# Kernel tuning notes

Measured on AMD Instinct MI355X. Metric: run time of the kernel, lower is better.

## Reference

```python
import jax, jax.numpy as jnp
import numpy as np

MASK_ID = 3
MAX_SEN = 128
SEN_DIM = 128
EMBED = 1024


def setup_inputs() -> dict:
    key = jax.random.key(0)
    ks = jax.random.split(key, 12)
    B, S, E, D = 8, 8192, EMBED, SEN_DIM
    s = 0.02
    return {
        "input_ids": jax.random.randint(ks[0], (B, S), 0, 64),
        "hidden_states": jax.random.normal(ks[1], (B, S, E), jnp.float32),
        "Wv": jax.random.normal(ks[2], (E, D), jnp.float32) * s,
        "bv": jnp.zeros((D,), jnp.float32),
        "Wq": jax.random.normal(ks[3], (E, D), jnp.float32) * s,
        "bq": jnp.zeros((D,), jnp.float32),
        "Wk": jax.random.normal(ks[4], (D, D), jnp.float32) * s,
        "bk": jnp.zeros((D,), jnp.float32),
        "Wvt": jax.random.normal(ks[5], (D, D), jnp.float32) * s,
        "bvt": jnp.zeros((D,), jnp.float32),
        "Wo": jax.random.normal(ks[6], (D, E), jnp.float32) * s,
        "bo": jnp.zeros((E,), jnp.float32),
    }


def reference(input_ids, hidden_states, Wv, bv, Wq, bq, Wk, bk, Wvt, bvt, Wo, bo):
    B, S, E = hidden_states.shape
    dt = hidden_states.dtype

    # sentence segmentation: each mask token t with running count c belongs to bucket c-1
    mask = input_ids == MASK_ID                               # (B, S)
    csum = jnp.cumsum(mask.astype(jnp.int32), axis=1)         # (B, S)
    # tokens that are not mask tokens (or overflow max_sen_num) go to dummy bucket MAX_SEN
    seg = jnp.where(mask & (csum <= MAX_SEN), csum - 1, MAX_SEN)  # (B, S)

    # segment-sum replacement for torch.bmm(sen_pos_mask, hidden_states)
    b_idx = jnp.arange(B)[:, None]
    pooled = jnp.zeros((B, MAX_SEN + 1, E), dt).at[b_idx, seg].add(hidden_states)[:, :MAX_SEN]  # (B, M, E)

    static_sen_states = pooled @ Wv + bv                      # (B, M, 128)

    q_token = (hidden_states @ Wq + bq) * (SEN_DIM ** -0.5)   # (B, S, 128)
    k_sen = static_sen_states @ Wk + bk                       # (B, M, 128)
    v_sen = static_sen_states @ Wvt + bvt                     # (B, M, 128)

    # token t may attend to sentences 0..csum[t]-1
    tmp_mask = (jnp.arange(MAX_SEN)[None, None, :] + 1) <= csum[:, :, None]  # (B, S, M)
    neg = jnp.finfo(dt).min
    logits = jnp.einsum('bsd,bmd->bsm', q_token, k_sen) + jnp.where(tmp_mask, jnp.zeros((), dt), neg)
    attn = jax.nn.softmax(logits, axis=-1) * tmp_mask.astype(dt)  # (B, S, M)

    sen_attn_output = jnp.einsum('bsm,bmd->bsd', attn, v_sen) @ Wo + bo  # (B, S, E)
    return sen_attn_output
```

## Files before the change

kernel.cpp:

```cpp
#include <hip/hip_runtime.h>
#include <hip/hip_bf16.h>

#define MASK_ID 3
#define MAX_SEN 128
#define NB 8
#define SEQ 8192
#define EMB 1024
#define DIM 128

typedef __attribute__((ext_vector_type(8))) short short8v;
typedef __attribute__((ext_vector_type(4))) float f32x4;

#define MFMA(a, b, c) __builtin_amdgcn_mfma_f32_16x16x32_bf16(a, b, c, 0, 0, 0)

__device__ __forceinline__ short f2b(float x) {
    union { float f; unsigned u; } v; v.f = x;
    unsigned r = (v.u + 0x7FFFu + ((v.u >> 16) & 1u)) >> 16;
    return (short)r;
}

__device__ __forceinline__ unsigned cvtpk(float a, float b) {
    unsigned r;
    asm("v_cvt_pk_bf16_f32 %0, %1, %2" : "=v"(r) : "v"(a), "v"(b));
    return r;
}

__global__ __launch_bounds__(1024) void seg_kernel(const int* __restrict__ ids,
                                                   int* __restrict__ pos,
                                                   int* __restrict__ nvis) {
    int b = blockIdx.x;
    int tid = threadIdx.x;
    __shared__ int sc[1024];
    __shared__ int sc2[1024];
    const int PER = SEQ / 1024;
    int base = b * SEQ + tid * PER;

    int ids_l[PER];
    int cnt = 0;
    #pragma unroll
    for (int j = 0; j < PER; j++) {
        ids_l[j] = ids[base + j];
        cnt += (ids_l[j] == MASK_ID) ? 1 : 0;
    }
    if (tid < MAX_SEN) pos[b * MAX_SEN + tid] = -1;
    sc[tid] = cnt;
    __syncthreads();

    int* src = sc;
    int* dst = sc2;
    for (int off = 1; off < 1024; off <<= 1) {
        int v = src[tid];
        if (tid >= off) v += src[tid - off];
        dst[tid] = v;
        __syncthreads();
        int* t = src; src = dst; dst = t;
    }
    int incl = src[tid];
    int run = incl - cnt;

    #pragma unroll
    for (int j = 0; j < PER; j++) {
        if (ids_l[j] == MASK_ID) {
            run++;
            if (run <= MAX_SEN) pos[b * MAX_SEN + run - 1] = tid * PER + j;
        }
        int nv = run; if (nv > MAX_SEN) nv = MAX_SEN;
        nvis[base + j] = nv;
    }
}

__global__ __launch_bounds__(256) void prep_w(const float* __restrict__ Wq,
                                              const float* __restrict__ Wo,
                                              short* __restrict__ WqTt,
                                              short* __restrict__ WoTt) {
    int t = blockIdx.x * 256 + threadIdx.x;
    {
        int fid = t >> 6, lp = t & 63;
        int c = fid >> 4, ks = (fid >> 3) & 1, cf = fid & 7;
        int e0 = c * 64 + ks * 32 + (lp >> 4) * 8;
        int d = cf * 16 + (lp & 15);
        short8v v;
        #pragma unroll
        for (int j = 0; j < 8; j++) v[j] = f2b(Wq[(size_t)(e0 + j) * 128 + d]);
        *(short8v*)(WqTt + fid * 512 + lp * 8) = v;
    }
    {
        int fid = t >> 6, lp = t & 63;
        int ef = fid >> 2, kk = fid & 3;
        int e = ef * 16 + (lp & 15);
        int dd0 = kk * 32 + (lp >> 4) * 8;
        short8v v;
        #pragma unroll
        for (int j = 0; j < 8; j++) v[j] = f2b(Wo[(size_t)(dd0 + j) * 1024 + e]);
        *(short8v*)(WoTt + fid * 512 + lp * 8) = v;
    }
}

__global__ __launch_bounds__(128) void statkv_kernel(const float* __restrict__ hidden,
                                                     const float* __restrict__ Wv, const float* __restrict__ bv,
                                                     const float* __restrict__ Wk, const float* __restrict__ bk,
                                                     const float* __restrict__ Wvt, const float* __restrict__ bvt,
                                                     const int* __restrict__ pos,
                                                     short* __restrict__ k_t, short* __restrict__ vT_t) {
    int mg = blockIdx.x;
    int b  = blockIdx.y;
    int d  = threadIdx.x;
    __shared__ float h[4][1024];
    __shared__ float st[4][128];
    int m0 = mg * 4;

    #pragma unroll
    for (int j = 0; j < 4; j++) {
        int p = pos[b * MAX_SEN + m0 + j];
        const float* hp = hidden + ((size_t)b * SEQ + (p < 0 ? 0 : p)) * EMB;
        #pragma unroll
        for (int ii = 0; ii < 2; ii++) {
            float4 v = {0.f, 0.f, 0.f, 0.f};
            if (p >= 0) v = *(const float4*)(hp + ii * 512 + d * 4);
            *(float4*)&h[j][ii * 512 + d * 4] = v;
        }
    }
    __syncthreads();

    float a0 = 0.f, a1 = 0.f, a2 = 0.f, a3 = 0.f;
    for (int e = 0; e < 1024; e += 4) {
        float w0 = Wv[(size_t)e * 128 + d];
        float w1 = Wv[(size_t)(e + 1) * 128 + d];
        float w2 = Wv[(size_t)(e + 2) * 128 + d];
        float w3 = Wv[(size_t)(e + 3) * 128 + d];
        float4 h0 = *(const float4*)&h[0][e];
        float4 h1 = *(const float4*)&h[1][e];
        float4 h2 = *(const float4*)&h[2][e];
        float4 h3 = *(const float4*)&h[3][e];
        a0 += h0.x * w0 + h0.y * w1 + h0.z * w2 + h0.w * w3;
        a1 += h1.x * w0 + h1.y * w1 + h1.z * w2 + h1.w * w3;
        a2 += h2.x * w0 + h2.y * w1 + h2.z * w2 + h2.w * w3;
        a3 += h3.x * w0 + h3.y * w1 + h3.z * w2 + h3.w * w3;
    }
    float bvd = bv[d];
    st[0][d] = bvd + a0;
    st[1][d] = bvd + a1;
    st[2][d] = bvd + a2;
    st[3][d] = bvd + a3;
    __syncthreads();

    float k0 = 0.f, k1 = 0.f, k2 = 0.f, k3 = 0.f;
    float v0 = 0.f, v1 = 0.f, v2 = 0.f, v3 = 0.f;
    for (int e = 0; e < 128; e += 4) {
        float wk0 = Wk[(e) * 128 + d],     wk1 = Wk[(e + 1) * 128 + d];
        float wk2 = Wk[(e + 2) * 128 + d], wk3 = Wk[(e + 3) * 128 + d];
        float wv0 = Wvt[(e) * 128 + d],     wv1 = Wvt[(e + 1) * 128 + d];
        float wv2 = Wvt[(e + 2) * 128 + d], wv3 = Wvt[(e + 3) * 128 + d];
        float4 s0 = *(const float4*)&st[0][e];
        float4 s1 = *(const float4*)&st[1][e];
        float4 s2 = *(const float4*)&st[2][e];
        float4 s3 = *(const float4*)&st[3][e];
        k0 += s0.x * wk0 + s0.y * wk1 + s0.z * wk2 + s0.w * wk3;
        k1 += s1.x * wk0 + s1.y * wk1 + s1.z * wk2 + s1.w * wk3;
        k2 += s2.x * wk0 + s2.y * wk1 + s2.z * wk2 + s2.w * wk3;
        k3 += s3.x * wk0 + s3.y * wk1 + s3.z * wk2 + s3.w * wk3;
        v0 += s0.x * wv0 + s0.y * wv1 + s0.z * wv2 + s0.w * wv3;
        v1 += s1.x * wv0 + s1.y * wv1 + s1.z * wv2 + s1.w * wv3;
        v2 += s2.x * wv0 + s2.y * wv1 + s2.z * wv2 + s2.w * wv3;
        v3 += s3.x * wv0 + s3.y * wv1 + s3.z * wv2 + s3.w * wv3;
    }
    float kv[4] = {k0, k1, k2, k3};
    float vv[4] = {v0, v1, v2, v3};
    float bkd = bk[d], bvtd = bvt[d];
    #pragma unroll
    for (int j = 0; j < 4; j++) {
        int m = m0 + j;
        int kk = d >> 5, lq = (d >> 3) & 3, jj = d & 7;
        int fid = (m >> 4) * 4 + kk;
        k_t[(b << 14) + fid * 512 + (lq * 16 + (m & 15)) * 8 + jj] = f2b(bkd + kv[j]);
        int df = d >> 4, kk2 = m >> 5, lq2 = (m >> 3) & 3, j2 = m & 7;
        int fid2 = df * 4 + kk2;
        vT_t[(b << 14) + fid2 * 512 + (lq2 * 16 + (d & 15)) * 8 + j2] = f2b(bvtd + vv[j]);
    }
}

__global__ __launch_bounds__(256, 3) void attn_kernel(
    const float* __restrict__ hidden,
    const short* __restrict__ WqTt, const float* __restrict__ bq,
    const short* __restrict__ k_t, const short* __restrict__ vT_t,
    const short* __restrict__ WoTt, const float* __restrict__ bo,
    const int* __restrict__ nvis,
    float* __restrict__ out) {
    int wg = (blockIdx.x & 7) * 128 + (blockIdx.x >> 3);
    int b  = wg >> 7;
    int s0 = (wg & 127) * 64;
    int tid = threadIdx.x;
    int lane = tid & 63;
    int w  = tid >> 6;
    int lr = lane & 15;
    int lq = lane >> 4;

    __shared__ __align__(16) char SH[49152];
    char* Ab  = SH;
    char* pPc = SH;
    char* odc = SH + 16384;
    char* qPc = SH + 32768;

    const size_t hrow = (size_t)b * SEQ + s0;
    f32x4 zero = {0.f, 0.f, 0.f, 0.f};

    f32x4 acc[4][2];
    #pragma unroll
    for (int rf = 0; rf < 4; rf++) { acc[rf][0] = zero; acc[rf][1] = zero; }

    int rsub = tid >> 4;
    int cfl  = (tid & 15) * 4;
    const float* hA0 = hidden + (hrow + 0 * 16 + rsub) * EMB + cfl;
    const float* hA1 = hidden + (hrow + 1 * 16 + rsub) * EMB + cfl;
    const float* hA2 = hidden + (hrow + 2 * 16 + rsub) * EMB + cfl;
    const float* hA3 = hidden + (hrow + 3 * 16 + rsub) * EMB + cfl;
    int swzA = (rsub & 7) << 4;
    int dA0 = (0 * 16 + rsub) * 128 + (((tid & 15) * 8) ^ swzA);
    int dA1 = (1 * 16 + rsub) * 128 + (((tid & 15) * 8) ^ swzA);
    int dA2 = (2 * 16 + rsub) * 128 + (((tid & 15) * 8) ^ swzA);
    int dA3 = (3 * 16 + rsub) * 128 + (((tid & 15) * 8) ^ swzA);

    float4 pa0[4], pa1[4], pa2[4];
    short8v Wa[4], Wb[4];

#define LOADA(C, PA) do { \
    PA[0] = *(const float4*)(hA0 + (C) * 64); \
    PA[1] = *(const float4*)(hA1 + (C) * 64); \
    PA[2] = *(const float4*)(hA2 + (C) * 64); \
    PA[3] = *(const float4*)(hA3 + (C) * 64); } while (0)

#define LOADW(C, W) do { \
    const short* wp = WqTt + ((C) * 16 + 2 * w) * 512 + lane * 8; \
    W[0] = *(const short8v*)(wp); \
    W[1] = *(const short8v*)(wp + 512); \
    W[2] = *(const short8v*)(wp + 8 * 512); \
    W[3] = *(const short8v*)(wp + 9 * 512); } while (0)

#define STORE_A(PA) do { \
    unsigned long long v0_ = (unsigned long long)cvtpk(PA[0].z, PA[0].w) << 32 | cvtpk(PA[0].x, PA[0].y); \
    unsigned long long v1_ = (unsigned long long)cvtpk(PA[1].z, PA[1].w) << 32 | cvtpk(PA[1].x, PA[1].y); \
    unsigned long long v2_ = (unsigned long long)cvtpk(PA[2].z, PA[2].w) << 32 | cvtpk(PA[2].x, PA[2].y); \
    unsigned long long v3_ = (unsigned long long)cvtpk(PA[3].z, PA[3].w) << 32 | cvtpk(PA[3].x, PA[3].y); \
    *(unsigned long long*)(Ab + dA0) = v0_; \
    *(unsigned long long*)(Ab + dA1) = v1_; \
    *(unsigned long long*)(Ab + dA2) = v2_; \
    *(unsigned long long*)(Ab + dA3) = v3_; } while (0)

#define COMPUTE(W) do { \
    _Pragma("unroll") \
    for (int ks = 0; ks < 2; ks++) { \
        _Pragma("unroll") \
        for (int rf = 0; rf < 4; rf++) { \
            int row = rf * 16 + lr; \
            short8v fa = *(short8v*)(Ab + ((row * 128 + ks * 64 + lq * 16) ^ ((row & 7) << 4))); \
            acc[rf][0] = MFMA(fa, W[ks * 2 + 0], acc[rf][0]); \
            acc[rf][1] = MFMA(fa, W[ks * 2 + 1], acc[rf][1]); \
        } } } while (0)

#define ITER(c, PA, WW, DO_A, DO_W) do { \
    __builtin_amdgcn_s_barrier();                  \
    STORE_A(PA);                                   \
    if (DO_A) LOADA((c) + 3, PA); \
    asm volatile("s_waitcnt lgkmcnt(0)" ::: "memory"); \
    __builtin_amdgcn_sched_barrier(0); \
    __builtin_amdgcn_s_barrier();                  \
    COMPUTE(WW);                                   \
    if (DO_W) LOADW((c) + 2, WW);                  \
    } while (0)

    LOADW(0, Wa);
    LOADW(1, Wb);
    LOADA(0, pa0);
    LOADA(1, pa1);
    LOADA(2, pa2);

    ITER(0,  pa0, Wa, 1, 1);
    ITER(1,  pa1, Wb, 1, 1);
    ITER(2,  pa2, Wa, 1, 1);
    ITER(3,  pa0, Wb, 1, 1);
    ITER(4,  pa1, Wa, 1, 1);
    ITER(5,  pa2, Wb, 1, 1);
    ITER(6,  pa0, Wa, 1, 1);
    ITER(7,  pa1, Wb, 1, 1);
    ITER(8,  pa2, Wa, 1, 1);
    ITER(9,  pa0, Wb, 1, 1);
    ITER(10, pa1, Wa, 1, 1);
    ITER(11, pa2, Wb, 1, 1);
    ITER(12, pa0, Wa, 1, 1);
    ITER(13, pa1, Wb, 0, 1);
    ITER(14, pa2, Wa, 0, 0);
    ITER(15, pa0, Wb, 0, 0);

    {
        const float scale = 0.08838834764831845f;
        int d0 = w * 32 + lr;
        float bq0 = bq[d0], bq1 = bq[d0 + 16];
        #pragma unroll
        for (int rf = 0; rf < 4; rf++)
            #pragma unroll
            for (int r = 0; r < 4; r++) {
                int row = rf * 16 + lq * 4 + r;
                int x = (row & 7) << 4;
                *(short*)(qPc + row * 256 + ((d0 * 2) ^ x))        = f2b((acc[rf][0][r] + bq0) * scale);
                *(short*)(qPc + row * 256 + (((d0 + 16) * 2) ^ x)) = f2b((acc[rf][1][r] + bq1) * scale);
            }
    }
    __syncthreads();

    {
        f32x4 l[4][2];
        #pragma unroll
        for (int rf = 0; rf < 4; rf++) { l[rf][0] = zero; l[rf][1] = zero; }
        const short* kbase = k_t + (b << 14) + (2 * w) * 4 * 512 + lane * 8;
        #pragma unroll
        for (int kk = 0; kk < 4; kk++) {
            const short8v fb0 = *(const short8v*)(kbase + kk * 512);
            const short8v fb1 = *(const short8v*)(kbase + (4 + kk) * 512);
            #pragma unroll
            for (int rf = 0; rf < 4; rf++) {
                int row = rf * 16 + lr;
                int x = (row & 7) << 4;
                short8v fa = *(short8v*)(qPc + row * 256 + ((kk * 64 + lq * 16) ^ x));
                l[rf][0] = MFMA(fa, fb0, l[rf][0]);
                l[rf][1] = MFMA(fa, fb1, l[rf][1]);
            }
        }
        #pragma unroll
        for (int rf = 0; rf < 4; rf++)
            #pragma unroll
            for (int r = 0; r < 4; r++) {
                int row = rf * 16 + lq * 4 + r;
                int x = (row & 7) << 4;
                *(float*)(SH + row * 512 + (((w * 32 + lr) * 4) ^ x))      = l[rf][0][r];
                *(float*)(SH + row * 512 + (((w * 32 + 16 + lr) * 4) ^ x)) = l[rf][1][r];
            }
    }
    __syncthreads();

    {
        int t = tid >> 2, sub = tid & 3;
        int nv = nvis[b * SEQ + s0 + t];
        int x = (t & 7) << 4;
        float pv[32];
        #pragma unroll
        for (int u = 0; u < 8; u++) {
            float4 v = *(const float4*)(SH + t * 512 + ((sub * 128 + u * 16) ^ x));
            pv[u * 4]     = v.x; pv[u * 4 + 1] = v.y;
            pv[u * 4 + 2] = v.z; pv[u * 4 + 3] = v.w;
        }
        int base_m = sub * 32;
        float mx = -3.0e38f;
        #pragma unroll
        for (int i = 0; i < 32; i++)
            mx = (base_m + i < nv) ? fmaxf(mx, pv[i]) : mx;
        mx = fmaxf(mx, __shfl_xor(mx, 1));
        mx = fmaxf(mx, __shfl_xor(mx, 2));
        float sum = 0.f;
        #pragma unroll
        for (int i = 0; i < 32; i++) {
            float e = (base_m + i < nv) ? __expf(pv[i] - mx) : 0.f;
            pv[i] = e;
            sum += e;
        }
        sum += __shfl_xor(sum, 1);
        sum += __shfl_xor(sum, 2);
        float inv = (nv > 0) ? 1.0f / sum : 0.f;

        __syncthreads();

        #pragma unroll
        for (int u = 0; u < 4; u++) {
            union { short8v s; unsigned uu[4]; } p;
            #pragma unroll
            for (int i = 0; i < 4; i++)
                p.uu[i] = cvtpk(pv[u * 8 + 2 * i] * inv, pv[u * 8 + 2 * i + 1] * inv);
            *(short8v*)(pPc + t * 256 + ((sub * 64 + u * 16) ^ x)) = p.s;
        }
    }
    __syncthreads();

    {
        f32x4 o[4][2];
        #pragma unroll
        for (int rf = 0; rf < 4; rf++) { o[rf][0] = zero; o[rf][1] = zero; }
        const short* vbase = vT_t + (b << 14) + (2 * w) * 4 * 512 + lane * 8;
        #pragma unroll
        for (int kk = 0; kk < 4; kk++) {
            const short8v fb0 = *(const short8v*)(vbase + kk * 512);
            const short8v fb1 = *(const short8v*)(vbase + (4 + kk) * 512);
            #pragma unroll
            for (int rf = 0; rf < 4; rf++) {
                int row = rf * 16 + lr;
                int x = (row & 7) << 4;
                short8v fa = *(short8v*)(pPc + row * 256 + ((kk * 64 + lq * 16) ^ x));
                o[rf][0] = MFMA(fa, fb0, o[rf][0]);
                o[rf][1] = MFMA(fa, fb1, o[rf][1]);
            }
        }
        int d0 = w * 32 + lr;
        #pragma unroll
        for (int rf = 0; rf < 4; rf++)
            #pragma unroll
            for (int r = 0; r < 4; r++) {
                int row = rf * 16 + lq * 4 + r;
                int x = (row & 7) << 4;
                *(short*)(odc + row * 256 + ((d0 * 2) ^ x))        = f2b(o[rf][0][r]);
                *(short*)(odc + row * 256 + (((d0 + 16) * 2) ^ x)) = f2b(o[rf][1][r]);
            }
    }
    __syncthreads();

    {
        short8v af[4][4];
        #pragma unroll
        for (int rf = 0; rf < 4; rf++)
            #pragma unroll
            for (int kk = 0; kk < 4; kk++) {
                int row = rf * 16 + lr;
                int x = (row & 7) << 4;
                af[rf][kk] = *(short8v*)(odc + row * 256 + ((kk * 64 + lq * 16) ^ x));
            }
        __syncthreads();

        float* cst = (float*)SH;
        int srow2 = tid >> 4;
        int scidx = (tid & 15) * 4;

        #pragma unroll
        for (int grp = 0; grp < 4; grp++) {
            f32x4 ac[4][4];
            #pragma unroll
            for (int rf = 0; rf < 4; rf++)
                #pragma unroll
                for (int cf = 0; cf < 4; cf++) ac[rf][cf] = zero;
            #pragma unroll
            for (int kk = 0; kk < 4; kk++) {
                #pragma unroll
                for (int cf = 0; cf < 4; cf++) {
                    const short8v bb = *(const short8v*)(WoTt
                        + ((grp * 16 + w * 4 + cf) * 4 + kk) * 512 + lane * 8);
                    #pragma unroll
                    for (int rf = 0; rf < 4; rf++)
                        ac[rf][cf] = MFMA(af[rf][kk], bb, ac[rf][cf]);
                }
            }
            #pragma unroll
            for (int rf = 0; rf < 4; rf++) {
                #pragma unroll
                for (int cf = 0; cf < 4; cf++)
                    #pragma unroll
                    for (int r = 0; r < 4; r++)
                        cst[(lq * 4 + r) * 260 + w * 64 + cf * 16 + lr] = ac[rf][cf][r];
                __syncthreads();
                #pragma unroll
                for (int i = 0; i < 4; i++) {
                    int cidx = scidx + i * 64;
                    float4 v = *(const float4*)(cst + srow2 * 260 + cidx);
                    float4 b4 = *(const float4*)(bo + grp * 256 + cidx);
                    v.x += b4.x; v.y += b4.y; v.z += b4.z; v.w += b4.w;
                    *(float4*)(&out[(hrow + rf * 16 + srow2) * EMB + grp * 256 + cidx]) = v;
                }
                __syncthreads();
            }
        }
    }
}

extern "C" void kernel_launch(void* const* d_in, const int* in_sizes, int n_in,
                              void* d_out, int out_size, void* d_ws, size_t ws_size,
                              hipStream_t stream) {
    const int*   ids    = (const int*)d_in[0];
    const float* hidden = (const float*)d_in[1];
    const float* Wv     = (const float*)d_in[2];
    const float* bv     = (const float*)d_in[3];
    const float* Wq     = (const float*)d_in[4];
    const float* bq     = (const float*)d_in[5];
    const float* Wk     = (const float*)d_in[6];
    const float* bk     = (const float*)d_in[7];
    const float* Wvt    = (const float*)d_in[8];
    const float* bvt    = (const float*)d_in[9];
    const float* Wo     = (const float*)d_in[10];
    const float* bo     = (const float*)d_in[11];

    char* ws = (char*)d_ws;
    int*   pos   = (int*)ws;
    int*   nvis  = (int*)(ws + (4 << 10));
    short* k_t   = (short*)(ws + (260 << 10));
    short* vT_t  = (short*)(ws + (516 << 10));
    short* WqTt  = (short*)(ws + (772 << 10));
    short* WoTt  = (short*)(ws + (1028 << 10));

    seg_kernel<<<NB, 1024, 0, stream>>>(ids, pos, nvis);
    prep_w<<<64, 256, 0, stream>>>(Wq, Wo, WqTt, WoTt);
    dim3 g2(32, NB);
    statkv_kernel<<<g2, 128, 0, stream>>>(hidden, Wv, bv, Wk, bk, Wvt, bvt, pos, k_t, vT_t);
    attn_kernel<<<NB * (SEQ / 64), 256, 0, stream>>>(hidden, WqTt, bq, k_t, vT_t, WoTt, bo,
                                                     nvis, (float*)d_out);
}
```

Before: 217.2 us.

## Merge seg/prep kernels, widen statkv rows, triple-buffer Q-projection LDS tiles

Folds the weight-conversion kernel into the segmentation kernel with extra blocks, which saves one launch. The statkv kernel now handles 8 sentences per block instead of 4, halving its grid and reusing each weight load across more rows. In the attention kernel, the Q-projection A tile moves from a single LDS buffer to three rotating buffers with one barrier per iteration instead of two. This gives more prefetch distance and less synchronisation, at the cost of more LDS and more register pressure.

```diff
diff --git a/kernel.cpp b/kernel.cpp
--- a/kernel.cpp
+++ b/kernel.cpp
@@ -25,74 +25,75 @@
     return r;
 }
 
-__global__ __launch_bounds__(1024) void seg_kernel(const int* __restrict__ ids,
-                                                   int* __restrict__ pos,
-                                                   int* __restrict__ nvis) {
-    int b = blockIdx.x;
-    int tid = threadIdx.x;
+__global__ __launch_bounds__(1024) void seg_prep_kernel(const int* __restrict__ ids,
+                                                        int* __restrict__ pos,
+                                                        int* __restrict__ nvis,
+                                                        const float* __restrict__ Wq,
+                                                        const float* __restrict__ Wo,
+                                                        short* __restrict__ WqTt,
+                                                        short* __restrict__ WoTt) {
     __shared__ int sc[1024];
     __shared__ int sc2[1024];
-    const int PER = SEQ / 1024;
-    int base = b * SEQ + tid * PER;
-
-    int ids_l[PER];
-    int cnt = 0;
-    #pragma unroll
-    for (int j = 0; j < PER; j++) {
-        ids_l[j] = ids[base + j];
-        cnt += (ids_l[j] == MASK_ID) ? 1 : 0;
-    }
-    if (tid < MAX_SEN) pos[b * MAX_SEN + tid] = -1;
-    sc[tid] = cnt;
-    __syncthreads();
-
-    int* src = sc;
-    int* dst = sc2;
-    for (int off = 1; off < 1024; off <<= 1) {
-        int v = src[tid];
-        if (tid >= off) v += src[tid - off];
-        dst[tid] = v;
+    int tid = threadIdx.x;
+    if (blockIdx.x < 8) {
+        int b = blockIdx.x;
+        const int PER = SEQ / 1024;
+        int base = b * SEQ + tid * PER;
+
+        int ids_l[PER];
+        int cnt = 0;
+        #pragma unroll
+        for (int j = 0; j < PER; j++) {
+            ids_l[j] = ids[base + j];
+            cnt += (ids_l[j] == MASK_ID) ? 1 : 0;
+        }
+        if (tid < MAX_SEN) pos[b * MAX_SEN + tid] = -1;
+        sc[tid] = cnt;
         __syncthreads();
-        int* t = src; src = dst; dst = t;
-    }
-    int incl = src[tid];
-    int run = incl - cnt;
-
-    #pragma unroll
-    for (int j = 0; j < PER; j++) {
-        if (ids_l[j] == MASK_ID) {
-            run++;
-            if (run <= MAX_SEN) pos[b * MAX_SEN + run - 1] = tid * PER + j;
-        }
-        int nv = run; if (nv > MAX_SEN) nv = MAX_SEN;
-        nvis[base + j] = nv;
-    }
-}
-
-__global__ __launch_bounds__(256) void prep_w(const float* __restrict__ Wq,
-                                              const float* __restrict__ Wo,
-                                              short* __restrict__ WqTt,
-                                              short* __restrict__ WoTt) {
-    int t = blockIdx.x * 256 + threadIdx.x;
-    {
-        int fid = t >> 6, lp = t & 63;
-        int c = fid >> 4, ks = (fid >> 3) & 1, cf = fid & 7;
-        int e0 = c * 64 + ks * 32 + (lp >> 4) * 8;
-        int d = cf * 16 + (lp & 15);
-        short8v v;
-        #pragma unroll
-        for (int j = 0; j < 8; j++) v[j] = f2b(Wq[(size_t)(e0 + j) * 128 + d]);
-        *(short8v*)(WqTt + fid * 512 + lp * 8) = v;
-    }
-    {
-        int fid = t >> 6, lp = t & 63;
-        int ef = fid >> 2, kk = fid & 3;
-        int e = ef * 16 + (lp & 15);
-        int dd0 = kk * 32 + (lp >> 4) * 8;
-        short8v v;
-        #pragma unroll
-        for (int j = 0; j < 8; j++) v[j] = f2b(Wo[(size_t)(dd0 + j) * 1024 + e]);
-        *(short8v*)(WoTt + fid * 512 + lp * 8) = v;
+
+        int* src = sc;
+        int* dst = sc2;
+        for (int off = 1; off < 1024; off <<= 1) {
+            int v = src[tid];
+            if (tid >= off) v += src[tid - off];
+            dst[tid] = v;
+            __syncthreads();
+            int* t = src; src = dst; dst = t;
+        }
+        int incl = src[tid];
+        int run = incl - cnt;
+
+        #pragma unroll
+        for (int j = 0; j < PER; j++) {
+            if (ids_l[j] == MASK_ID) {
+                run++;
+                if (run <= MAX_SEN) pos[b * MAX_SEN + run - 1] = tid * PER + j;
+            }
+            int nv = run; if (nv > MAX_SEN) nv = MAX_SEN;
+            nvis[base + j] = nv;
+        }
+    } else {
+        int t = (blockIdx.x - 8) * 1024 + tid;
+        {
+            int fid = t >> 6, lp = t & 63;
+            int c = fid >> 4, ks = (fid >> 3) & 1, cf = fid & 7;
+            int e0 = c * 64 + ks * 32 + (lp >> 4) * 8;
+            int d = cf * 16 + (lp & 15);
+            short8v v;
+            #pragma unroll
+            for (int j = 0; j < 8; j++) v[j] = f2b(Wq[(size_t)(e0 + j) * 128 + d]);
+            *(short8v*)(WqTt + fid * 512 + lp * 8) = v;
+        }
+        {
+            int fid = t >> 6, lp = t & 63;
+            int ef = fid >> 2, kk = fid & 3;
+            int e = ef * 16 + (lp & 15);
+            int dd0 = kk * 32 + (lp >> 4) * 8;
+            short8v v;
+            #pragma unroll
+            for (int j = 0; j < 8; j++) v[j] = f2b(Wo[(size_t)(dd0 + j) * 1024 + e]);
+            *(short8v*)(WoTt + fid * 512 + lp * 8) = v;
+        }
     }
 }
 
@@ -105,12 +106,12 @@
     int mg = blockIdx.x;
     int b  = blockIdx.y;
     int d  = threadIdx.x;
-    __shared__ float h[4][1024];
-    __shared__ float st[4][128];
-    int m0 = mg * 4;
-
-    #pragma unroll
-    for (int j = 0; j < 4; j++) {
+    __shared__ float h[8][1024];
+    __shared__ float st[8][128];
+    int m0 = mg * 8;
+
+    #pragma unroll
+    for (int j = 0; j < 8; j++) {
         int p = pos[b * MAX_SEN + m0 + j];
         const float* hp = hidden + ((size_t)b * SEQ + (p < 0 ? 0 : p)) * EMB;
         #pragma unroll
@@ -122,53 +123,41 @@
     }
     __syncthreads();
 
-    float a0 = 0.f, a1 = 0.f, a2 = 0.f, a3 = 0.f;
+    float a[8];
+    #pragma unroll
+    for (int j = 0; j < 8; j++) a[j] = 0.f;
     for (int e = 0; e < 1024; e += 4) {
         float w0 = Wv[(size_t)e * 128 + d];
         float w1 = Wv[(size_t)(e + 1) * 128 + d];
         float w2 = Wv[(size_t)(e + 2) * 128 + d];
         float w3 = Wv[(size_t)(e + 3) * 128 + d];
-        float4 h0 = *(const float4*)&h[0][e];
-        float4 h1 = *(const float4*)&h[1][e];
-        float4 h2 = *(const float4*)&h[2][e];
-        float4 h3 = *(const float4*)&h[3][e];
-        a0 += h0.x * w0 + h0.y * w1 + h0.z * w2 + h0.w * w3;
-        a1 += h1.x * w0 + h1.y * w1 + h1.z * w2 + h1.w * w3;
-        a2 += h2.x * w0 + h2.y * w1 + h2.z * w2 + h2.w * w3;
-        a3 += h3.x * w0 + h3.y * w1 + h3.z * w2 + h3.w * w3;
+        #pragma unroll
+        for (int j = 0; j < 8; j++) {
+            float4 hj = *(const float4*)&h[j][e];
+            a[j] += hj.x * w0 + hj.y * w1 + hj.z * w2 + hj.w * w3;
+        }
     }
     float bvd = bv[d];
-    st[0][d] = bvd + a0;
-    st[1][d] = bvd + a1;
-    st[2][d] = bvd + a2;
-    st[3][d] = bvd + a3;
-    __syncthreads();
-
-    float k0 = 0.f, k1 = 0.f, k2 = 0.f, k3 = 0.f;
-    float v0 = 0.f, v1 = 0.f, v2 = 0.f, v3 = 0.f;
-    for (int e = 0; e < 128; e += 4) {
-        float wk0 = Wk[(e) * 128 + d],     wk1 = Wk[(e + 1) * 128 + d];
-        float wk2 = Wk[(e + 2) * 128 + d], wk3 = Wk[(e + 3) * 128 + d];
-        float wv0 = Wvt[(e) * 128 + d],     wv1 = Wvt[(e + 1) * 128 + d];
-        float wv2 = Wvt[(e + 2) * 128 + d], wv3 = Wvt[(e + 3) * 128 + d];
-        float4 s0 = *(const float4*)&st[0][e];
-        float4 s1 = *(const float4*)&st[1][e];
-        float4 s2 = *(const float4*)&st[2][e];
-        float4 s3 = *(const float4*)&st[3][e];
-        k0 += s0.x * wk0 + s0.y * wk1 + s0.z * wk2 + s0.w * wk3;
-        k1 += s1.x * wk0 + s1.y * wk1 + s1.z * wk2 + s1.w * wk3;
-        k2 += s2.x * wk0 + s2.y * wk1 + s2.z * wk2 + s2.w * wk3;
-        k3 += s3.x * wk0 + s3.y * wk1 + s3.z * wk2 + s3.w * wk3;
-        v0 += s0.x * wv0 + s0.y * wv1 + s0.z * wv2 + s0.w * wv3;
-        v1 += s1.x * wv0 + s1.y * wv1 + s1.z * wv2 + s1.w * wv3;
-        v2 += s2.x * wv0 + s2.y * wv1 + s2.z * wv2 + s2.w * wv3;
-        v3 += s3.x * wv0 + s3.y * wv1 + s3.z * wv2 + s3.w * wv3;
-    }
-    float kv[4] = {k0, k1, k2, k3};
-    float vv[4] = {v0, v1, v2, v3};
+    #pragma unroll
+    for (int j = 0; j < 8; j++) st[j][d] = bvd + a[j];
+    __syncthreads();
+
+    float kv[8], vv[8];
+    #pragma unroll
+    for (int j = 0; j < 8; j++) { kv[j] = 0.f; vv[j] = 0.f; }
+    for (int e = 0; e < 128; e += 2) {
+        float wk0 = Wk[(e) * 128 + d],  wk1 = Wk[(e + 1) * 128 + d];
+        float wv0 = Wvt[(e) * 128 + d], wv1 = Wvt[(e + 1) * 128 + d];
+        #pragma unroll
+        for (int j = 0; j < 8; j++) {
+            float s0 = st[j][e], s1 = st[j][e + 1];
+            kv[j] += s0 * wk0 + s1 * wk1;
+            vv[j] += s0 * wv0 + s1 * wv1;
+        }
+    }
     float bkd = bk[d], bvtd = bvt[d];
     #pragma unroll
-    for (int j = 0; j < 4; j++) {
+    for (int j = 0; j < 8; j++) {
         int m = m0 + j;
         int kk = d >> 5, lq = (d >> 3) & 3, jj = d & 7;
         int fid = (m >> 4) * 4 + kk;
@@ -196,7 +185,9 @@
     int lq = lane >> 4;
 
     __shared__ __align__(16) char SH[49152];
-    char* Ab  = SH;
+    char* Ab0 = SH;
+    char* Ab1 = SH + 8192;
+    char* Ab2 = SH + 16384;
     char* pPc = SH;
     char* odc = SH + 16384;
     char* qPc = SH + 32768;
@@ -236,35 +227,34 @@
     W[2] = *(const short8v*)(wp + 8 * 512); \
     W[3] = *(const short8v*)(wp + 9 * 512); } while (0)
 
-#define STORE_A(PA) do { \
+#define STORE_A(PA, AB) do { \
     unsigned long long v0_ = (unsigned long long)cvtpk(PA[0].z, PA[0].w) << 32 | cvtpk(PA[0].x, PA[0].y); \
     unsigned long long v1_ = (unsigned long long)cvtpk(PA[1].z, PA[1].w) << 32 | cvtpk(PA[1].x, PA[1].y); \
     unsigned long long v2_ = (unsigned long long)cvtpk(PA[2].z, PA[2].w) << 32 | cvtpk(PA[2].x, PA[2].y); \
     unsigned long long v3_ = (unsigned long long)cvtpk(PA[3].z, PA[3].w) << 32 | cvtpk(PA[3].x, PA[3].y); \
-    *(unsigned long long*)(Ab + dA0) = v0_; \
-    *(unsigned long long*)(Ab + dA1) = v1_; \
-    *(unsigned long long*)(Ab + dA2) = v2_; \
-    *(unsigned long long*)(Ab + dA3) = v3_; } while (0)
-
-#define COMPUTE(W) do { \
+    *(unsigned long long*)((AB) + dA0) = v0_; \
+    *(unsigned long long*)((AB) + dA1) = v1_; \
+    *(unsigned long long*)((AB) + dA2) = v2_; \
+    *(unsigned long long*)((AB) + dA3) = v3_; } while (0)
+
+#define COMPUTE(AB, W) do { \
     _Pragma("unroll") \
     for (int ks = 0; ks < 2; ks++) { \
         _Pragma("unroll") \
         for (int rf = 0; rf < 4; rf++) { \
             int row = rf * 16 + lr; \
-            short8v fa = *(short8v*)(Ab + ((row * 128 + ks * 64 + lq * 16) ^ ((row & 7) << 4))); \
+            short8v fa = *(short8v*)((AB) + ((row * 128 + ks * 64 + lq * 16) ^ ((row & 7) << 4))); \
             acc[rf][0] = MFMA(fa, W[ks * 2 + 0], acc[rf][0]); \
             acc[rf][1] = MFMA(fa, W[ks * 2 + 1], acc[rf][1]); \
         } } } while (0)
 
-#define ITER(c, PA, WW, DO_A, DO_W) do { \
-    __builtin_amdgcn_s_barrier();                  \
-    STORE_A(PA);                                   \
-    if (DO_A) LOADA((c) + 3, PA); \
+#define ITER(c, PAn, BUFn, BUFc, WW, DO_A, DO_W) do { \
+    STORE_A(PAn, BUFn);                            \
+    if (DO_A) LOADA((c) + 4, PAn); \
     asm volatile("s_waitcnt lgkmcnt(0)" ::: "memory"); \
     __builtin_amdgcn_sched_barrier(0); \
     __builtin_amdgcn_s_barrier();                  \
-    COMPUTE(WW);                                   \
+    COMPUTE(BUFc, WW);                             \
     if (DO_W) LOADW((c) + 2, WW);                  \
     } while (0)
 
@@ -273,23 +263,28 @@
     LOADA(0, pa0);
     LOADA(1, pa1);
     LOADA(2, pa2);
-
-    ITER(0,  pa0, Wa, 1, 1);
-    ITER(1,  pa1, Wb, 1, 1);
-    ITER(2,  pa2, Wa, 1, 1);
-    ITER(3,  pa0, Wb, 1, 1);
-    ITER(4,  pa1, Wa, 1, 1);
-    ITER(5,  pa2, Wb, 1, 1);
-    ITER(6,  pa0, Wa, 1, 1);
-    ITER(7,  pa1, Wb, 1, 1);
-    ITER(8,  pa2, Wa, 1, 1);
-    ITER(9,  pa0, Wb, 1, 1);
-    ITER(10, pa1, Wa, 1, 1);
-    ITER(11, pa2, Wb, 1, 1);
-    ITER(12, pa0, Wa, 1, 1);
-    ITER(13, pa1, Wb, 0, 1);
-    ITER(14, pa2, Wa, 0, 0);
-    ITER(15, pa0, Wb, 0, 0);
+    STORE_A(pa0, Ab0);
+    LOADA(3, pa0);
+    asm volatile("s_waitcnt lgkmcnt(0)" ::: "memory");
+    __builtin_amdgcn_sched_barrier(0);
+    __builtin_amdgcn_s_barrier();
+
+    ITER(0,  pa1, Ab1, Ab0, Wa, 1, 1);
+    ITER(1,  pa2, Ab2, Ab1, Wb, 1, 1);
+    ITER(2,  pa0, Ab0, Ab2, Wa, 1, 1);
+    ITER(3,  pa1, Ab1, Ab0, Wb, 1, 1);
+    ITER(4,  pa2, Ab2, Ab1, Wa, 1, 1);
+    ITER(5,  pa0, Ab0, Ab2, Wb, 1, 1);
+    ITER(6,  pa1, Ab1, Ab0, Wa, 1, 1);
+    ITER(7,  pa2, Ab2, Ab1, Wb, 1, 1);
+    ITER(8,  pa0, Ab0, Ab2, Wa, 1, 1);
+    ITER(9,  pa1, Ab1, Ab0, Wb, 1, 1);
+    ITER(10, pa2, Ab2, Ab1, Wa, 1, 1);
+    ITER(11, pa0, Ab0, Ab2, Wb, 1, 1);
+    ITER(12, pa1, Ab1, Ab0, Wa, 0, 1);
+    ITER(13, pa2, Ab2, Ab1, Wb, 0, 1);
+    ITER(14, pa0, Ab0, Ab2, Wa, 0, 0);
+    COMPUTE(Ab0, Wb);
 
     {
         const float scale = 0.08838834764831845f;
@@ -490,9 +485,8 @@
     short* WqTt  = (short*)(ws + (772 << 10));
     short* WoTt  = (short*)(ws + (1028 << 10));
 
-    seg_kernel<<<NB, 1024, 0, stream>>>(ids, pos, nvis);
-    prep_w<<<64, 256, 0, stream>>>(Wq, Wo, WqTt, WoTt);
-    dim3 g2(32, NB);
+    seg_prep_kernel<<<24, 1024, 0, stream>>>(ids, pos, nvis, Wq, Wo, WqTt, WoTt);
+    dim3 g2(16, NB);
     statkv_kernel<<<g2, 128, 0, stream>>>(hidden, Wv, bv, Wk, bk, Wvt, bvt, pos, k_t, vT_t);
     attn_kernel<<<NB * (SEQ / 64), 256, 0, stream>>>(hidden, WqTt, bq, k_t, vT_t, WoTt, bo,
                                                      nvis, (float*)d_out);
```

Measured after the change: 252.5 us. 16.2% more time.
